# Kernel optimization log

Measured on AMD Instinct MI355X. Metric: run time of the kernel, lower is better.

The kernel has to match this reference:

```python
import jax, jax.numpy as jnp
import numpy as np

TOPK = 5
EPS = 1e-8  # torch CosineSimilarity eps


def setup_inputs() -> dict:
    key = jax.random.key(0)
    k1, k2, k3 = jax.random.split(key, 3)
    B, N, D, L = 64, 100000, 768, 32
    query = jax.random.normal(k1, (B, D), dtype=jnp.float32)
    knowledge_embed = jax.random.normal(k2, (N, D), dtype=jnp.float32)
    knowledge_full = jax.random.randint(k3, (N, L), 0, 30000, dtype=jnp.int32)
    return {"query": query, "knowledge_embed": knowledge_embed, "knowledge_full": knowledge_full}


def reference(query, knowledge_embed, knowledge_full):
    # Batched cosine similarity: [B, N]
    q_norm = jnp.linalg.norm(query, axis=-1, keepdims=True)            # [B, 1]
    k_norm = jnp.linalg.norm(knowledge_embed, axis=-1, keepdims=True)  # [N, 1]
    dots = jnp.einsum("bd,nd->bn", query, knowledge_embed)             # [B, N]
    denom = jnp.maximum(q_norm * k_norm.T, EPS)                        # [B, N]
    sims = dots / denom
    # topk over knowledge axis
    _, indices = jax.lax.top_k(sims, TOPK)                             # [B, topk]
    topk_embed = knowledge_embed[indices]                              # [B, topk, D]
    topk_knowledge = knowledge_full[indices]                           # [B, topk, L]
    return (topk_knowledge, topk_embed)
```

## Files before the change

### kernel.cpp

```cpp
#include <hip/hip_runtime.h>
#include <cfloat>
#include <climits>


#define BQ 64
#define DD 768
#define NK 100000
#define LK 32
#define K_TOP 5
#define TROWS 16
#define NTIL (NK / TROWS)
#define NBLKS 512
#define T_CAND 16

typedef __attribute__((ext_vector_type(8))) short short8;
typedef __attribute__((ext_vector_type(4))) float f32x4;

static __device__ __forceinline__ ushort bf16_rtn(float x) {
    uint u = __float_as_uint(x);
    return (ushort)((u + 0x7FFFu + ((u >> 16) & 1u)) >> 16);
}

#define INS8(v, n, va, ia)                                                  \
    _Pragma("unroll")                                                       \
    for (int m_ = 0; m_ < 8; ++m_) {                                        \
        if ((v) > va[m_]) {                                                 \
            float tv_ = va[m_]; va[m_] = (v); (v) = tv_;                    \
            int ti_ = ia[m_]; ia[m_] = (n); (n) = ti_;                      \
        }                                                                   \
    }

__global__ __launch_bounds__(256) void prep_kernel(const float* __restrict__ q,
                                                   ushort* __restrict__ qf,
                                                   float* __restrict__ qn) {
    const int b = blockIdx.x, t = threadIdx.x;
    __shared__ float red[4];
    float v[3];
    float s = 0.f;
#pragma unroll
    for (int i = 0; i < 3; ++i) {
        v[i] = q[b * DD + t + i * 256];
        s = fmaf(v[i], v[i], s);
    }
    for (int off = 32; off > 0; off >>= 1) s += __shfl_down(s, off, 64);
    if ((t & 63) == 0) red[t >> 6] = s;
    __syncthreads();
    const float tot = red[0] + red[1] + red[2] + red[3];
    const float rq = rsqrtf(tot);
    const int qb = b >> 4, bi = b & 15;
#pragma unroll
    for (int i = 0; i < 3; ++i) {
        const int k = t + i * 256;
        const int kt = k >> 5, lg = (k >> 3) & 3, j = k & 7;
        qf[((size_t)(kt * 4 + qb) * 64 + lg * 16 + bi) * 8 + j] = bf16_rtn(v[i] * rq);
    }
    if (t == 0) qn[b] = sqrtf(tot);
}

__global__ __launch_bounds__(256) void sims_kernel(const ushort* __restrict__ qf,
                                                   const float* __restrict__ ke,
                                                   float2* __restrict__ pv) {
    __shared__ ushort Bb[TROWS * DD];
    __shared__ float  S[BQ][17];

    const int t = threadIdx.x;
    const int w = t >> 6, l = t & 63;
    const int lg = l >> 4, li = l & 15;
    const int qd = t & 63, jq = t >> 6;

    float v8[8]; int i8[8];
#pragma unroll
    for (int m = 0; m < 8; ++m) { v8[m] = -FLT_MAX; i8[m] = INT_MAX; }

    f32x4 sr[4][3];
    int tile = blockIdx.x;

    {
        const float* g = ke + (size_t)(tile * TROWS + w * 4) * DD + l * 4;
#pragma unroll
        for (int i = 0; i < 4; ++i)
#pragma unroll
            for (int c = 0; c < 3; ++c)
                sr[i][c] = *(const f32x4*)(g + i * DD + c * 256);
    }

    const ushort* aq = qf + (size_t)w * 512 + l * 8;
    short8 A[24];
#pragma unroll
    for (int p = 0; p < 24; ++p) A[p] = *(const short8*)(aq + p * 2048);

    while (true) {
        const int nxt = tile + NBLKS;

        char* bb = (char*)Bb;
#pragma unroll
        for (int i = 0; i < 4; ++i) {
            const int row = w * 4 + i;
            const int base = row * 1536 + l * 8;
            const int sw = (row & 7) << 4;
#pragma unroll
            for (int c = 0; c < 3; ++c) {
                uint2 u;
                u.x = __builtin_amdgcn_perm(__float_as_uint(sr[i][c][1]),
                                            __float_as_uint(sr[i][c][0]),
                                            0x07060302u);
                u.y = __builtin_amdgcn_perm(__float_as_uint(sr[i][c][3]),
                                            __float_as_uint(sr[i][c][2]),
                                            0x07060302u);
                *(uint2*)(bb + ((base + c * 512) ^ sw)) = u;
            }
        }
        if (nxt < NTIL) {
            const float* g = ke + (size_t)(nxt * TROWS + w * 4) * DD + l * 4;
#pragma unroll
            for (int i = 0; i < 4; ++i)
#pragma unroll
                for (int c = 0; c < 3; ++c)
                    sr[i][c] = *(const f32x4*)(g + i * DD + c * 256);
        }
        asm volatile("s_waitcnt lgkmcnt(0)" ::: "memory");
        __builtin_amdgcn_sched_barrier(0);
        __builtin_amdgcn_s_barrier();
        __builtin_amdgcn_sched_barrier(0);

        const int boff = li * 1536 + lg * 16;
        const int bsw = (li & 7) << 4;
        f32x4 acc = (f32x4){0.f, 0.f, 0.f, 0.f};
        f32x4 ncc = (f32x4){0.f, 0.f, 0.f, 0.f};
        short8 br[2];
        br[0] = *(const short8*)(bb + (boff ^ bsw));
#pragma unroll
        for (int kt = 0; kt < 24; ++kt) {
            const int cb = kt & 1;
            if (kt < 23)
                br[cb ^ 1] = *(const short8*)(bb + ((boff + (kt + 1) * 64) ^ bsw));
            acc = __builtin_amdgcn_mfma_f32_16x16x32_bf16(A[kt], br[cb], acc, 0, 0, 0);
            ncc = __builtin_amdgcn_mfma_f32_16x16x32_bf16(br[cb], br[cb], ncc, 0, 0, 0);
        }

        float x = ncc[li & 3];
        float dsq = __shfl(x, ((li >> 2) << 4) | li, 64);
        float rk = rsqrtf(dsq);

#pragma unroll
        for (int r = 0; r < 4; ++r) S[w * 16 + lg * 4 + r][li] = acc[r] * rk;
        asm volatile("s_waitcnt lgkmcnt(0)" ::: "memory");
        __builtin_amdgcn_sched_barrier(0);
        __builtin_amdgcn_s_barrier();
        __builtin_amdgcn_sched_barrier(0);

        {
            const int nb = tile * TROWS + jq * 4;
#pragma unroll
            for (int j = 0; j < 4; ++j) {
                float v = S[qd][jq * 4 + j]; int n = nb + j;
                INS8(v, n, v8, i8);
            }
        }
        if (nxt >= NTIL) break;
        tile = nxt;
    }

    __syncthreads();
    float2* mg = (float2*)(&Bb[0]);
#pragma unroll
    for (int m = 0; m < 8; ++m) mg[t * 8 + m] = make_float2(v8[m], __int_as_float(i8[m]));
    __syncthreads();
    if (t < BQ) {
        float vf[8]; int nf[8];
#pragma unroll
        for (int m = 0; m < 8; ++m) { vf[m] = -FLT_MAX; nf[m] = INT_MAX; }
        for (int s = 0; s < 4; ++s) {
            const float2* rowp = &mg[(t + s * 64) * 8];
#pragma unroll
            for (int m = 0; m < 8; ++m) {
                float v = rowp[m].x; int n = __float_as_int(rowp[m].y);
                INS8(v, n, vf, nf);
            }
        }
        float2* dst = pv + ((size_t)t * NBLKS + blockIdx.x) * 8;
#pragma unroll
        for (int m = 0; m < 8; ++m) dst[m] = make_float2(vf[m], __int_as_float(nf[m]));
    }
}

__global__ __launch_bounds__(256) void merge_rescore_kernel(
    const float2* __restrict__ pv,
    const float* __restrict__ q, const float* __restrict__ ke,
    const int* __restrict__ kf, const float* __restrict__ qn,
    float* __restrict__ out) {
    const int qi = blockIdx.x, t = threadIdx.x;
    __shared__ float sv[256][8];
    __shared__ int   si[256][8];
    __shared__ int   ci[T_CAND];
    __shared__ float cs_[T_CAND];
    __shared__ int   fi[K_TOP];

    float v8[8]; int i8[8];
#pragma unroll
    for (int m = 0; m < 8; ++m) { v8[m] = -FLT_MAX; i8[m] = INT_MAX; }

    const float2* src = pv + (size_t)qi * NBLKS * 8;
#pragma unroll 4
    for (int c = t; c < NBLKS * 8; c += 256) {
        float2 e = src[c];
        float v = e.x; int n = __float_as_int(e.y);
        INS8(v, n, v8, i8);
    }
#pragma unroll
    for (int m = 0; m < 8; ++m) { sv[t][m] = v8[m]; si[t][m] = i8[m]; }
    __syncthreads();

    for (int active = 64; active >= 4; active >>= 2) {
        if (t < active) {
#pragma unroll
            for (int m = 0; m < 8; ++m) { v8[m] = -FLT_MAX; i8[m] = INT_MAX; }
            for (int s = 0; s < 4; ++s) {
                int row = t * 4 + s;
#pragma unroll
                for (int m = 0; m < 8; ++m) {
                    float v = sv[row][m]; int n = si[row][m];
                    INS8(v, n, v8, i8);
                }
            }
        }
        __syncthreads();
        if (t < active) {
#pragma unroll
            for (int m = 0; m < 8; ++m) { sv[t][m] = v8[m]; si[t][m] = i8[m]; }
        }
        __syncthreads();
    }

    if (t == 0) {
        float v16[T_CAND]; int i16[T_CAND];
#pragma unroll
        for (int m = 0; m < T_CAND; ++m) { v16[m] = -FLT_MAX; i16[m] = INT_MAX; }
        for (int row = 0; row < 4; ++row) {
#pragma unroll
            for (int m = 0; m < 8; ++m) {
                float v = sv[row][m]; int n = si[row][m];
#pragma unroll
                for (int p = 0; p < T_CAND; ++p) {
                    if (v > v16[p]) {
                        float tv = v16[p]; v16[p] = v; v = tv;
                        int ti = i16[p]; i16[p] = n; n = ti;
                    }
                }
            }
        }
#pragma unroll
        for (int m = 0; m < T_CAND; ++m) ci[m] = i16[m];
    }
    __syncthreads();

    {
        const int w = t >> 6, lane = t & 63;
        for (int cc = 0; cc < 4; ++cc) {
            int c = w * 4 + cc;
            int row = ci[c];
            const float* kp = ke + (size_t)row * DD + lane * 12;
            const float* qp = q + qi * DD + lane * 12;
            float d = 0.f, ks = 0.f;
#pragma unroll
            for (int i = 0; i < 12; ++i) {
                float kv = kp[i];
                d = fmaf(qp[i], kv, d);
                ks = fmaf(kv, kv, ks);
            }
#pragma unroll
            for (int off = 32; off > 0; off >>= 1) {
                d += __shfl_xor(d, off, 64);
                ks += __shfl_xor(ks, off, 64);
            }
            if (lane == 0)
                cs_[c] = d / fmaxf(qn[qi] * sqrtf(ks), 1e-8f);
        }
    }
    __syncthreads();

    if (t == 0) {
        float v5[K_TOP]; int i5[K_TOP];
#pragma unroll
        for (int m = 0; m < K_TOP; ++m) { v5[m] = -FLT_MAX; i5[m] = INT_MAX; }
        for (int c = 0; c < T_CAND; ++c) {
            float v = cs_[c]; int n = ci[c];
#pragma unroll
            for (int m = 0; m < K_TOP; ++m) {
                bool take = (v > v5[m]) || (v == v5[m] && n < i5[m]);
                if (take) {
                    float tv = v5[m]; v5[m] = v; v = tv;
                    int ti = i5[m]; i5[m] = n; n = ti;
                }
            }
        }
#pragma unroll
        for (int m = 0; m < K_TOP; ++m) fi[m] = i5[m];
    }
    __syncthreads();

    for (int pos = t; pos < K_TOP * LK; pos += 256) {
        int m = pos >> 5, lgi = pos & 31;
        out[(qi * K_TOP + m) * LK + lgi] = (float)kf[(size_t)fi[m] * LK + lgi];
    }
    const int EO = BQ * K_TOP * LK;
    for (int m = 0; m < K_TOP; ++m) {
        const float4* srcp = (const float4*)(ke + (size_t)fi[m] * DD);
        float4* dstp = (float4*)(out + EO + (size_t)(qi * K_TOP + m) * DD);
        for (int pos = t; pos < DD / 4; pos += 256) dstp[pos] = srcp[pos];
    }
}

extern "C" void kernel_launch(void* const* d_in, const int* in_sizes, int n_in,
                              void* d_out, int out_size, void* d_ws, size_t ws_size,
                              hipStream_t stream) {
    const float* query = (const float*)d_in[0];
    const float* ke    = (const float*)d_in[1];
    const int*   kf    = (const int*)d_in[2];
    float* out = (float*)d_out;

    float2* pv = (float2*)d_ws;
    ushort* qf = (ushort*)((char*)d_ws + (size_t)BQ * NBLKS * 8 * sizeof(float2));
    float*  qn = (float*)((char*)qf + (size_t)24 * 4 * 64 * 8 * sizeof(ushort));

    prep_kernel<<<BQ, 256, 0, stream>>>(query, qf, qn);
    sims_kernel<<<NBLKS, 256, 0, stream>>>(qf, ke, pv);
    merge_rescore_kernel<<<BQ, 256, 0, stream>>>(pv, query, ke, kf, qn, out);
}
```

Before: 145.5 us.

## Stream fp32 embeddings directly to LDS with double-buffered global_load_lds

Replaces the register-staged load, bf16 pack and LDS store of each 16-row embedding tile with direct global-to-LDS async loads into a double-buffered fp32 tile. The bf16 conversion moves into the MFMA inner loop, which now reads fp32 from LDS. The next tile's load is issued before computing on the current one, aiming to overlap HBM traffic with compute and cut register pressure. Grid size is halved to 256 blocks. LDS footprint doubles (two fp32 buffers), LDS read volume per MFMA doubles, and the perm work sits on the MFMA critical path.

```diff
diff --git a/kernel.cpp b/kernel.cpp
--- a/kernel.cpp
+++ b/kernel.cpp
@@ -10,7 +10,7 @@
 #define K_TOP 5
 #define TROWS 16
 #define NTIL (NK / TROWS)
-#define NBLKS 512
+#define NBLKS 256
 #define T_CAND 16
 
 typedef __attribute__((ext_vector_type(8))) short short8;
@@ -19,6 +19,13 @@
 static __device__ __forceinline__ ushort bf16_rtn(float x) {
     uint u = __float_as_uint(x);
     return (ushort)((u + 0x7FFFu + ((u >> 16) & 1u)) >> 16);
+}
+
+static __device__ __forceinline__ void gload_lds16(const float* gsrc, float* ldsdst) {
+    __builtin_amdgcn_global_load_lds(
+        (const __attribute__((address_space(1))) unsigned int*)gsrc,
+        (__attribute__((address_space(3))) unsigned int*)ldsdst,
+        16, 0, 0);
 }
 
 #define INS8(v, n, va, ia)                                                  \
@@ -60,8 +67,8 @@
 __global__ __launch_bounds__(256) void sims_kernel(const ushort* __restrict__ qf,
                                                    const float* __restrict__ ke,
                                                    float2* __restrict__ pv) {
-    __shared__ ushort Bb[TROWS * DD];
-    __shared__ float  S[BQ][17];
+    __shared__ float Bf[2][TROWS * DD];
+    __shared__ float S[BQ][17];
 
     const int t = threadIdx.x;
     const int w = t >> 6, l = t & 63;
@@ -72,18 +79,24 @@
 #pragma unroll
     for (int m = 0; m < 8; ++m) { v8[m] = -FLT_MAX; i8[m] = INT_MAX; }
 
-    f32x4 sr[4][3];
+#define ISSUE(tl, buf) do {                                                 \
+        _Pragma("unroll")                                                   \
+        for (int i_ = 0; i_ < 4; ++i_) {                                    \
+            const int r_ = w * 4 + i_;                                      \
+            const float* gr_ = ke + (size_t)((tl) * TROWS + r_) * DD;       \
+            const int swb_ = (r_ & 7) << 4;                                 \
+            const int lf_ = ((l * 16) ^ swb_) >> 2;                         \
+            float* ld_ = &Bf[buf][r_ * DD];                                 \
+            _Pragma("unroll")                                               \
+            for (int c_ = 0; c_ < 3; ++c_)                                  \
+                gload_lds16(gr_ + c_ * 256 + lf_, ld_ + c_ * 256);          \
+        }                                                                   \
+    } while (0)
+
     int tile = blockIdx.x;
-
-    {
-        const float* g = ke + (size_t)(tile * TROWS + w * 4) * DD + l * 4;
-#pragma unroll
-        for (int i = 0; i < 4; ++i)
-#pragma unroll
-            for (int c = 0; c < 3; ++c)
-                sr[i][c] = *(const f32x4*)(g + i * DD + c * 256);
-    }
-
+    int cur = 0;
+
+    ISSUE(tile, 0);
     const ushort* aq = qf + (size_t)w * 512 + l * 8;
     short8 A[24];
 #pragma unroll
@@ -92,50 +105,48 @@
     while (true) {
         const int nxt = tile + NBLKS;
 
-        char* bb = (char*)Bb;
-#pragma unroll
-        for (int i = 0; i < 4; ++i) {
-            const int row = w * 4 + i;
-            const int base = row * 1536 + l * 8;
-            const int sw = (row & 7) << 4;
-#pragma unroll
-            for (int c = 0; c < 3; ++c) {
-                uint2 u;
-                u.x = __builtin_amdgcn_perm(__float_as_uint(sr[i][c][1]),
-                                            __float_as_uint(sr[i][c][0]),
-                                            0x07060302u);
-                u.y = __builtin_amdgcn_perm(__float_as_uint(sr[i][c][3]),
-                                            __float_as_uint(sr[i][c][2]),
-                                            0x07060302u);
-                *(uint2*)(bb + ((base + c * 512) ^ sw)) = u;
-            }
-        }
+        __builtin_amdgcn_sched_barrier(0);
         if (nxt < NTIL) {
-            const float* g = ke + (size_t)(nxt * TROWS + w * 4) * DD + l * 4;
-#pragma unroll
-            for (int i = 0; i < 4; ++i)
-#pragma unroll
-                for (int c = 0; c < 3; ++c)
-                    sr[i][c] = *(const f32x4*)(g + i * DD + c * 256);
-        }
-        asm volatile("s_waitcnt lgkmcnt(0)" ::: "memory");
+            ISSUE(nxt, cur ^ 1);
+            __builtin_amdgcn_sched_barrier(0);
+            asm volatile("s_waitcnt vmcnt(12)" ::: "memory");
+        } else {
+            asm volatile("s_waitcnt vmcnt(0)" ::: "memory");
+        }
         __builtin_amdgcn_sched_barrier(0);
         __builtin_amdgcn_s_barrier();
         __builtin_amdgcn_sched_barrier(0);
 
-        const int boff = li * 1536 + lg * 16;
-        const int bsw = (li & 7) << 4;
+        const char* bb = (const char*)&Bf[cur][0];
+        const int rowb = li * 3072;
+        const int sw = (li & 7) << 4;
         f32x4 acc = (f32x4){0.f, 0.f, 0.f, 0.f};
         f32x4 ncc = (f32x4){0.f, 0.f, 0.f, 0.f};
-        short8 br[2];
-        br[0] = *(const short8*)(bb + (boff ^ bsw));
+        f32x4 b0[2], b1[2];
+        {
+            const int y = lg * 32;
+            b0[0] = *(const f32x4*)(bb + rowb + (y ^ sw));
+            b1[0] = *(const f32x4*)(bb + rowb + ((y + 16) ^ sw));
+        }
 #pragma unroll
         for (int kt = 0; kt < 24; ++kt) {
             const int cb = kt & 1;
-            if (kt < 23)
-                br[cb ^ 1] = *(const short8*)(bb + ((boff + (kt + 1) * 64) ^ bsw));
-            acc = __builtin_amdgcn_mfma_f32_16x16x32_bf16(A[kt], br[cb], acc, 0, 0, 0);
-            ncc = __builtin_amdgcn_mfma_f32_16x16x32_bf16(br[cb], br[cb], ncc, 0, 0, 0);
+            if (kt < 23) {
+                const int y = (kt + 1) * 128 + lg * 32;
+                b0[cb ^ 1] = *(const f32x4*)(bb + rowb + (y ^ sw));
+                b1[cb ^ 1] = *(const f32x4*)(bb + rowb + ((y + 16) ^ sw));
+            }
+            union { short8 s8; uint u[4]; } pk;
+            pk.u[0] = __builtin_amdgcn_perm(__float_as_uint(b0[cb][1]),
+                                            __float_as_uint(b0[cb][0]), 0x07060302u);
+            pk.u[1] = __builtin_amdgcn_perm(__float_as_uint(b0[cb][3]),
+                                            __float_as_uint(b0[cb][2]), 0x07060302u);
+            pk.u[2] = __builtin_amdgcn_perm(__float_as_uint(b1[cb][1]),
+                                            __float_as_uint(b1[cb][0]), 0x07060302u);
+            pk.u[3] = __builtin_amdgcn_perm(__float_as_uint(b1[cb][3]),
+                                            __float_as_uint(b1[cb][2]), 0x07060302u);
+            acc = __builtin_amdgcn_mfma_f32_16x16x32_bf16(A[kt], pk.s8, acc, 0, 0, 0);
+            ncc = __builtin_amdgcn_mfma_f32_16x16x32_bf16(pk.s8, pk.s8, ncc, 0, 0, 0);
         }
 
         float x = ncc[li & 3];
@@ -158,11 +169,12 @@
             }
         }
         if (nxt >= NTIL) break;
-        tile = nxt;
-    }
-
-    __syncthreads();
-    float2* mg = (float2*)(&Bb[0]);
+        tile = nxt; cur ^= 1;
+    }
+#undef ISSUE
+
+    __syncthreads();
+    float2* mg = (float2*)(&Bf[0][0]);
 #pragma unroll
     for (int m = 0; m < 8; ++m) mg[t * 8 + m] = make_float2(v8[m], __int_as_float(i8[m]));
     __syncthreads();
```

Result: slower. 184.2 us (+26.5%).

## Double-buffer LDS tile, use per-wave score scratch, drop block barrier, add early-reject top-k

Applied to the files above, without the earlier changes.

Double-buffers the bf16 key tile in shared memory and gives each wave its own score scratch, so the per-tile block-wide barrier can be removed. Each wave now keeps top-8 for its own 16 queries, and the final per-block merge is re-indexed to match. Insertions into the sorted top-8 are guarded by a comparison against the current minimum, both in the sims kernel and in the merge kernel. Launch bounds request two blocks per SIMD. The risk is that shared-memory usage doubles and that removing the barrier relies on the double buffer alone to keep waves from overwriting a tile others still read.

```diff
diff --git a/kernel.cpp b/kernel.cpp
--- a/kernel.cpp
+++ b/kernel.cpp
@@ -57,42 +57,43 @@
     if (t == 0) qn[b] = sqrtf(tot);
 }
 
-__global__ __launch_bounds__(256) void sims_kernel(const ushort* __restrict__ qf,
-                                                   const float* __restrict__ ke,
-                                                   float2* __restrict__ pv) {
-    __shared__ ushort Bb[TROWS * DD];
-    __shared__ float  S[BQ][17];
+__global__ __launch_bounds__(256, 2) void sims_kernel(const ushort* __restrict__ qf,
+                                                      const float* __restrict__ ke,
+                                                      float2* __restrict__ pv) {
+    __shared__ ushort Bb[2][TROWS * DD];
+    __shared__ float  Sw[4][16][17];
 
     const int t = threadIdx.x;
     const int w = t >> 6, l = t & 63;
     const int lg = l >> 4, li = l & 15;
-    const int qd = t & 63, jq = t >> 6;
+    const int sq = l & 15, sj = l >> 4;
 
     float v8[8]; int i8[8];
 #pragma unroll
     for (int m = 0; m < 8; ++m) { v8[m] = -FLT_MAX; i8[m] = INT_MAX; }
 
     f32x4 sr[4][3];
-    int tile = blockIdx.x;
+    const int b = blockIdx.x;
 
     {
-        const float* g = ke + (size_t)(tile * TROWS + w * 4) * DD + l * 4;
+        const float* g = ke + (size_t)(b * TROWS + w * 4) * DD + l * 4;
 #pragma unroll
         for (int i = 0; i < 4; ++i)
 #pragma unroll
             for (int c = 0; c < 3; ++c)
                 sr[i][c] = *(const f32x4*)(g + i * DD + c * 256);
     }
-
     const ushort* aq = qf + (size_t)w * 512 + l * 8;
     short8 A[24];
 #pragma unroll
     for (int p = 0; p < 24; ++p) A[p] = *(const short8*)(aq + p * 2048);
 
-    while (true) {
+    for (int k = 0; k < 13; ++k) {
+        const int tile = b + k * NBLKS;
+        if (tile >= NTIL) break;
         const int nxt = tile + NBLKS;
 
-        char* bb = (char*)Bb;
+        char* bb = (char*)(&Bb[k & 1][0]);
 #pragma unroll
         for (int i = 0; i < 4; ++i) {
             const int row = w * 4 + i;
@@ -143,26 +144,22 @@
         float rk = rsqrtf(dsq);
 
 #pragma unroll
-        for (int r = 0; r < 4; ++r) S[w * 16 + lg * 4 + r][li] = acc[r] * rk;
+        for (int r = 0; r < 4; ++r) Sw[w][lg * 4 + r][li] = acc[r] * rk;
         asm volatile("s_waitcnt lgkmcnt(0)" ::: "memory");
         __builtin_amdgcn_sched_barrier(0);
-        __builtin_amdgcn_s_barrier();
-        __builtin_amdgcn_sched_barrier(0);
 
         {
-            const int nb = tile * TROWS + jq * 4;
+            const int nb = tile * TROWS + sj * 4;
 #pragma unroll
             for (int j = 0; j < 4; ++j) {
-                float v = S[qd][jq * 4 + j]; int n = nb + j;
-                INS8(v, n, v8, i8);
-            }
-        }
-        if (nxt >= NTIL) break;
-        tile = nxt;
-    }
-
-    __syncthreads();
-    float2* mg = (float2*)(&Bb[0]);
+                float v = Sw[w][sq][sj * 4 + j];
+                if (v > v8[7]) { int n = nb + j; INS8(v, n, v8, i8); }
+            }
+        }
+    }
+
+    __syncthreads();
+    float2* mg = (float2*)(&Bb[0][0]);
 #pragma unroll
     for (int m = 0; m < 8; ++m) mg[t * 8 + m] = make_float2(v8[m], __int_as_float(i8[m]));
     __syncthreads();
@@ -170,8 +167,9 @@
         float vf[8]; int nf[8];
 #pragma unroll
         for (int m = 0; m < 8; ++m) { vf[m] = -FLT_MAX; nf[m] = INT_MAX; }
+        const int wq = t >> 4, iq = t & 15;
         for (int s = 0; s < 4; ++s) {
-            const float2* rowp = &mg[(t + s * 64) * 8];
+            const float2* rowp = &mg[(wq * 64 + iq + 16 * s) * 8];
 #pragma unroll
             for (int m = 0; m < 8; ++m) {
                 float v = rowp[m].x; int n = __float_as_int(rowp[m].y);
@@ -205,7 +203,7 @@
     for (int c = t; c < NBLKS * 8; c += 256) {
         float2 e = src[c];
         float v = e.x; int n = __float_as_int(e.y);
-        INS8(v, n, v8, i8);
+        if (v > v8[7]) { INS8(v, n, v8, i8); }
     }
 #pragma unroll
     for (int m = 0; m < 8; ++m) { sv[t][m] = v8[m]; si[t][m] = i8[m]; }
```

New measurement: 144.7 us. No clear change (-0.6%).
